# Kernel optimization log

Hardware: AMD Instinct MI355X
Metric: run time of the kernel (lower is better)

The kernel has to match this reference:

```python
import jax, jax.numpy as jnp
import numpy as np
import math

B, N, H, D = 2, 2048, 16, 64

def setup_inputs() -> dict:
    key = jax.random.key(0)
    kq, kk, kv = jax.random.split(key, 3)
    q = jax.random.normal(kq, (B, N, H, D), dtype=jnp.float32)
    k = jax.random.normal(kk, (B, N, H, D), dtype=jnp.float32)
    v = jax.random.normal(kv, (B, N, H, D), dtype=jnp.float32)
    return {"q": q, "k": k, "v": v}

def reference(q, k, v):
    d = q.shape[-1]
    # [b,n,h,d] -> [b,h,n,d]
    qh = jnp.transpose(q, (0, 2, 1, 3))
    kh = jnp.transpose(k, (0, 2, 1, 3))
    vh = jnp.transpose(v, (0, 2, 1, 3))
    # scores: [b,h,n,n]
    scores = jnp.einsum('bhqd,bhkd->bhqk', qh, kh) / math.sqrt(d)
    # jax.nn.softmax performs the stable max-subtraction internally,
    # matching the original's explicit max-subtract + softmax.
    attn = jax.nn.softmax(scores, axis=-1)
    o = jnp.einsum('bhqk,bhkd->bhqd', attn, vh)
    # back to [b,n,h,d]
    return jnp.transpose(o, (0, 2, 1, 3))
```

## Files before the change

### kernel.cpp

```cpp
#include <hip/hip_runtime.h>


typedef float  f32x4  __attribute__((ext_vector_type(4)));
typedef float  f32x16 __attribute__((ext_vector_type(16)));
typedef short  s16x8  __attribute__((ext_vector_type(8)));
typedef short  s16x4  __attribute__((ext_vector_type(4)));
typedef int    i32x4  __attribute__((ext_vector_type(4)));

#define QSCALE 0.18033688011112042f

__device__ __forceinline__ unsigned short bf16r(float f) {
    unsigned u = __builtin_bit_cast(unsigned, f);
    u += 0x7fffu + ((u >> 16) & 1u);
    return (unsigned short)(u >> 16);
}

__device__ __forceinline__ s16x8 cvt8f(const float* p) {
    f32x4 a = *(const f32x4*)p;
    f32x4 b = *(const f32x4*)(p + 4);
    s16x8 r;
#pragma unroll
    for (int i = 0; i < 4; ++i) { r[i] = (short)bf16r(a[i]); r[i+4] = (short)bf16r(b[i]); }
    return r;
}

__device__ __forceinline__ s16x8 cvt8f_scaled(const float* p, float s) {
    f32x4 a = *(const f32x4*)p;
    f32x4 b = *(const f32x4*)(p + 4);
    s16x8 r;
#pragma unroll
    for (int i = 0; i < 4; ++i) {
        r[i]   = (short)bf16r(a[i] * s);
        r[i+4] = (short)bf16r(b[i] * s);
    }
    return r;
}

__device__ __forceinline__ void gll16(const unsigned short* g, short* l) {
    __builtin_amdgcn_global_load_lds(
        (const __attribute__((address_space(1))) unsigned int*)g,
        (__attribute__((address_space(3))) unsigned int*)l, 16, 0, 0);
}

__device__ __forceinline__ int pack2(float lo, float hi) {
    unsigned ul = __builtin_bit_cast(unsigned, lo) + 0x8000u;
    unsigned uh = __builtin_bit_cast(unsigned, hi) + 0x8000u;
    return (int)__builtin_amdgcn_perm(uh, ul, 0x07060302u);
}

__global__ void __launch_bounds__(256)
prep(const float* __restrict__ K, const float* __restrict__ V,
     unsigned short* __restrict__ Kb, unsigned short* __restrict__ Vt) {
    const int t = threadIdx.x, bid = blockIdx.x;
    {
        size_t i = ((size_t)bid * 256 + t) * 16;
        *(s16x8*)(Kb + i)     = cvt8f(K + i);
        *(s16x8*)(Kb + i + 8) = cvt8f(K + i + 8);
    }
    __shared__ short tile[64 * 72];
    const int bh = bid & 31, nb = bid >> 5;
    const int b = bh >> 4, h = bh & 15;
    {
        const int l16 = t & 15, r = t >> 4;
#pragma unroll
        for (int p = 0; p < 4; ++p) {
            const int nl = p * 16 + r;
            const float* vp = V + ((size_t)(b * 2048 + nb * 64 + nl)) * 1024 + h * 64 + l16 * 4;
            f32x4 x = *(const f32x4*)vp;
#pragma unroll
            for (int i = 0; i < 4; ++i)
                tile[(l16 * 4 + i) * 72 + nl] = (short)bf16r(x[i]);
        }
    }
    __syncthreads();
    {
        const int s = t & 7, d0 = t >> 3;
#pragma unroll
        for (int p = 0; p < 2; ++p) {
            const int d = p * 32 + d0;
            s16x8 x = *(const s16x8*)&tile[d * 72 + s * 8];
            *(s16x8*)(Vt + ((size_t)(bh * 64 + d)) * 2048 + nb * 64 + s * 8) = x;
        }
    }
}

__global__ void __launch_bounds__(256, 2)
attn_fwd(const float* __restrict__ Q, const unsigned short* __restrict__ Kb,
         const unsigned short* __restrict__ Vt, float* __restrict__ O)
{
    __shared__ __align__(16) char smem[65536];

    const int t = threadIdx.x;
    const int w = t >> 6, lane = t & 63;
    const int g = lane >> 5, nl = lane & 31;
    const int qsel = w & 1, ksel = w >> 1;

    const int bid = blockIdx.x;
    const int bh  = bid & 31, qb = bid >> 5;
    const int b   = bh >> 4,  h  = bh & 15;
    const int q0  = qb * 128 + qsel * 64;

    s16x8 qf[2][4];
#pragma unroll
    for (int qt = 0; qt < 2; ++qt) {
        const float* qp = Q + ((size_t)(b * 2048 + q0 + qt * 32 + nl)) * 1024
                            + h * 64 + g * 8;
#pragma unroll
        for (int kc = 0; kc < 4; ++kc)
            qf[qt][kc] = cvt8f_scaled(qp + kc * 16, QSCALE);
    }

    f32x16 oa[2][2] = {};
    float lp[2] = {0.f, 0.f};

    const int lr = lane >> 3, ls = lane & 7;
    int koff[4], voff[4];
#pragma unroll
    for (int i = 0; i < 4; ++i) {
        const int r = qsel * 32 + i * 8 + lr;
        const int c = (ls - r) & 7;
        koff[i] = r * 1024 + c * 8;
        voff[i] = r * 2048 + c * 8;
    }
    const unsigned short* gKh = Kb + (size_t)b * 2097152 + h * 64;
    const unsigned short* gVh = Vt + (size_t)bh * 131072;
    short* dK[2] = { (short*)(smem + (0 * 2 + ksel) * 8192) + qsel * 2048,
                     (short*)(smem + (1 * 2 + ksel) * 8192) + qsel * 2048 };
    short* dV[2] = { (short*)(smem + 32768 + (0 * 2 + ksel) * 8192) + qsel * 2048,
                     (short*)(smem + 32768 + (1 * 2 + ksel) * 8192) + qsel * 2048 };

    auto issue = [&](int it, int buf) {
        const int kb = ksel * 16 + it;
        const unsigned short* gk = gKh + (size_t)kb * 65536;
        const unsigned short* gv = gVh + kb * 64;
#pragma unroll
        for (int i = 0; i < 4; ++i) {
            gll16(gk + koff[i], dK[buf] + i * 512);
            gll16(gv + voff[i], dV[buf] + i * 512);
        }
    };

    issue(0, 0);

    for (int it = 0; it < 16; ++it) {
        const int cur = it & 1;
        __syncthreads();
        if (it + 1 < 16) issue(it + 1, cur ^ 1);

        const short* bK = (const short*)(smem + (cur * 2 + ksel) * 8192);
        const short* bV = (const short*)(smem + 32768 + (cur * 2 + ksel) * 8192);

        int pk[2][2][8];
#pragma unroll
        for (int kt = 0; kt < 2; ++kt) {
            s16x8 af[4];
#pragma unroll
            for (int kc = 0; kc < 4; ++kc) {
                const int row = kt * 32 + nl;
                af[kc] = *(const s16x8*)&bK[row * 64 + ((2 * kc + g + row) & 7) * 8];
            }
#pragma unroll
            for (int qt = 0; qt < 2; ++qt) {
                f32x16 s = {};
#pragma unroll
                for (int kc = 0; kc < 4; ++kc)
                    s = __builtin_amdgcn_mfma_f32_32x32x16_bf16(af[kc], qf[qt][kc], s, 0, 0, 0);
                float p[16];
#pragma unroll
                for (int r = 0; r < 16; ++r) {
                    p[r] = __builtin_amdgcn_exp2f(s[r]);
                    lp[qt] += p[r];
                }
#pragma unroll
                for (int i = 0; i < 8; ++i)
                    pk[kt][qt][i] = pack2(p[2 * i], p[2 * i + 1]);
            }
        }

#pragma unroll
        for (int dt = 0; dt < 2; ++dt) {
            const int row = dt * 32 + nl;
#pragma unroll
            for (int kt = 0; kt < 2; ++kt) {
#pragma unroll
                for (int s = 0; s < 2; ++s) {
                    s16x4 aL = *(const s16x4*)&bV[row * 64 + ((4 * kt + s     + row) & 7) * 8 + g * 4];
                    s16x4 aH = *(const s16x4*)&bV[row * 64 + ((4 * kt + 2 + s + row) & 7) * 8 + g * 4];
                    s16x8 a = __builtin_shufflevector(aL, aH, 0, 1, 2, 3, 4, 5, 6, 7);
#pragma unroll
                    for (int qt = 0; qt < 2; ++qt) {
                        i32x4 bd = { pk[kt][qt][s * 2], pk[kt][qt][s * 2 + 1],
                                     pk[kt][qt][s * 2 + 4], pk[kt][qt][s * 2 + 5] };
                        oa[dt][qt] = __builtin_amdgcn_mfma_f32_32x32x16_bf16(
                            a, __builtin_bit_cast(s16x8, bd), oa[dt][qt], 0, 0, 0);
                    }
                }
            }
        }
    }

    __syncthreads();
    float* ex = (float*)smem;
    float* zone = ex + qsel * 4224 + lane * 66;
    if (ksel) {
#pragma unroll
        for (int dt = 0; dt < 2; ++dt)
#pragma unroll
            for (int qt = 0; qt < 2; ++qt)
#pragma unroll
                for (int i = 0; i < 4; ++i)
                    *(f32x4*)(zone + (dt * 2 + qt) * 16 + i * 4) =
                        (f32x4){ oa[dt][qt][4*i], oa[dt][qt][4*i+1],
                                 oa[dt][qt][4*i+2], oa[dt][qt][4*i+3] };
        zone[64] = lp[0];
        zone[65] = lp[1];
    }
    __syncthreads();
    if (!ksel) {
#pragma unroll
        for (int dt = 0; dt < 2; ++dt)
#pragma unroll
            for (int qt = 0; qt < 2; ++qt)
#pragma unroll
                for (int i = 0; i < 4; ++i) {
                    f32x4 u = *(const f32x4*)(zone + (dt * 2 + qt) * 16 + i * 4);
#pragma unroll
                    for (int j = 0; j < 4; ++j) oa[dt][qt][4*i+j] += u[j];
                }
        float inv[2];
#pragma unroll
        for (int qt = 0; qt < 2; ++qt) {
            float s = lp[qt] + zone[64 + qt];
            s += __shfl_xor(s, 32);
            inv[qt] = 1.0f / s;
        }
#pragma unroll
        for (int qt = 0; qt < 2; ++qt) {
            float* op = O + ((size_t)(b * 2048 + q0 + qt * 32 + nl)) * 1024 + h * 64;
#pragma unroll
            for (int dt = 0; dt < 2; ++dt)
#pragma unroll
                for (int rq = 0; rq < 4; ++rq) {
                    const int d = dt * 32 + 8 * rq + 4 * g;
                    *(f32x4*)(op + d) = (f32x4){
                        oa[dt][qt][4*rq]   * inv[qt], oa[dt][qt][4*rq+1] * inv[qt],
                        oa[dt][qt][4*rq+2] * inv[qt], oa[dt][qt][4*rq+3] * inv[qt] };
                }
        }
    }
}

extern "C" void kernel_launch(void* const* d_in, const int* in_sizes, int n_in,
                              void* d_out, int out_size, void* d_ws, size_t ws_size,
                              hipStream_t stream) {
    const float* q = (const float*)d_in[0];
    const float* k = (const float*)d_in[1];
    const float* v = (const float*)d_in[2];
    float* o = (float*)d_out;

    unsigned short* Kb = (unsigned short*)d_ws;
    unsigned short* Vt = Kb + 4194304;

    hipLaunchKernelGGL(prep,     dim3(1024), dim3(256), 0, stream, k, v, Kb, Vt);
    hipLaunchKernelGGL(attn_fwd, dim3(512),  dim3(256), 0, stream, q, Kb, Vt, o);
}
```

Baseline: 135.9 us.

## Pre-tile and pre-swizzle K/V in prep so each wave streams private LDS buffers

The prep kernel now writes K and V as per-head contiguous 32-key tiles that are already in the swizzled LDS layout. Each wave then owns a private double-buffered LDS region, loads it with linear global_load_lds, and waits only on its own vmcnt, so the per-iteration block-wide __syncthreads disappears. The loop now processes 32-key steps (32 iterations) and hoists K/V fragment reads ahead of the next prefetch. It also vectorises the softmax row-sum accumulation. The risks are that waves loading the same key tiles now fetch them redundantly instead of sharing, and that an LDS buffer reused right after the vmcnt wait could race between waves.

After: 134.0 us. About the same (-1.4%).

```diff
diff --git a/kernel.cpp b/kernel.cpp
--- a/kernel.cpp
+++ b/kernel.cpp
@@ -50,42 +50,51 @@
 
 __global__ void __launch_bounds__(256)
 prep(const float* __restrict__ K, const float* __restrict__ V,
-     unsigned short* __restrict__ Kb, unsigned short* __restrict__ Vt) {
+     unsigned short* __restrict__ Kt, unsigned short* __restrict__ Vt) {
     const int t = threadIdx.x, bid = blockIdx.x;
-    {
-        size_t i = ((size_t)bid * 256 + t) * 16;
-        *(s16x8*)(Kb + i)     = cvt8f(K + i);
-        *(s16x8*)(Kb + i + 8) = cvt8f(K + i + 8);
-    }
-    __shared__ short tile[64 * 72];
     const int bh = bid & 31, nb = bid >> 5;
     const int b = bh >> 4, h = bh & 15;
+    const size_t tile0 = ((size_t)bh * 64 + nb * 2) * 2048;
+
+#pragma unroll
+    for (int i = 0; i < 2; ++i) {
+        const int lin = t * 2 + i;
+        const int kbl = lin >> 8, rem = lin & 255;
+        const int r = rem >> 3, s = rem & 7;
+        const int c = (s - r) & 7;
+        const float* src = K + ((size_t)(b * 2048 + nb * 64 + kbl * 32 + r)) * 1024
+                             + h * 64 + c * 8;
+        *(s16x8*)(Kt + tile0 + kbl * 2048 + r * 64 + s * 8) = cvt8f(src);
+    }
+
+    __shared__ short tile[64 * 72];
     {
         const int l16 = t & 15, r = t >> 4;
 #pragma unroll
         for (int p = 0; p < 4; ++p) {
-            const int nl = p * 16 + r;
-            const float* vp = V + ((size_t)(b * 2048 + nb * 64 + nl)) * 1024 + h * 64 + l16 * 4;
+            const int key = p * 16 + r;
+            const float* vp = V + ((size_t)(b * 2048 + nb * 64 + key)) * 1024
+                                + h * 64 + l16 * 4;
             f32x4 x = *(const f32x4*)vp;
 #pragma unroll
             for (int i = 0; i < 4; ++i)
-                tile[(l16 * 4 + i) * 72 + nl] = (short)bf16r(x[i]);
+                tile[(l16 * 4 + i) * 72 + key] = (short)bf16r(x[i]);
         }
     }
     __syncthreads();
-    {
-        const int s = t & 7, d0 = t >> 3;
-#pragma unroll
-        for (int p = 0; p < 2; ++p) {
-            const int d = p * 32 + d0;
-            s16x8 x = *(const s16x8*)&tile[d * 72 + s * 8];
-            *(s16x8*)(Vt + ((size_t)(bh * 64 + d)) * 2048 + nb * 64 + s * 8) = x;
-        }
+#pragma unroll
+    for (int i = 0; i < 4; ++i) {
+        const int lin = t * 4 + i;
+        const int kbl = lin >> 9, rem = lin & 511;
+        const int d = rem >> 3, p = rem & 7;
+        const int u = (p - (d >> 1)) & 7;
+        s16x4 x = *(const s16x4*)&tile[d * 72 + kbl * 32 + u * 4];
+        *(s16x4*)(Vt + tile0 + kbl * 2048 + d * 32 + p * 4) = x;
     }
 }
 
 __global__ void __launch_bounds__(256, 2)
-attn_fwd(const float* __restrict__ Q, const unsigned short* __restrict__ Kb,
+attn_fwd(const float* __restrict__ Q, const unsigned short* __restrict__ Kt,
          const unsigned short* __restrict__ Vt, float* __restrict__ O)
 {
     __shared__ __align__(16) char smem[65536];
@@ -100,6 +109,10 @@
     const int b   = bh >> 4,  h  = bh & 15;
     const int q0  = qb * 128 + qsel * 64;
 
+    char* wbase = smem + w * 16384;
+    short* sKb[2] = { (short*)wbase,            (short*)(wbase + 4096) };
+    short* sVb[2] = { (short*)(wbase + 8192),   (short*)(wbase + 12288) };
+
     s16x8 qf[2][4];
 #pragma unroll
     for (int qt = 0; qt < 2; ++qt) {
@@ -110,98 +123,98 @@
             qf[qt][kc] = cvt8f_scaled(qp + kc * 16, QSCALE);
     }
 
+    int koffr[4];
+#pragma unroll
+    for (int kc = 0; kc < 4; ++kc)
+        koffr[kc] = nl * 64 + ((2 * kc + g + nl) & 7) * 8;
+    int voffr[2][2];
+#pragma unroll
+    for (int s = 0; s < 2; ++s) {
+        voffr[s][0] = nl * 32 + (((2 * s + g)     + (nl >> 1)) & 7) * 4;
+        voffr[s][1] = nl * 32 + (((4 + 2 * s + g) + (nl >> 1)) & 7) * 4;
+    }
+
+    const int lane8 = lane * 8;
+    const unsigned short* gbase = Kt + (size_t)bh * 131072;
+    const unsigned short* vbase = Vt + (size_t)bh * 131072;
+
+    auto issue = [&](int it, int buf) {
+        const int kb = ksel * 32 + it;
+        const unsigned short* gk = gbase + (size_t)kb * 2048 + lane8;
+        const unsigned short* gv = vbase + (size_t)kb * 2048 + lane8;
+#pragma unroll
+        for (int i = 0; i < 4; ++i) {
+            gll16(gk + i * 512, sKb[buf] + i * 512);
+            gll16(gv + i * 512, sVb[buf] + i * 512);
+        }
+    };
+
+    issue(0, 0);
+
     f32x16 oa[2][2] = {};
-    float lp[2] = {0.f, 0.f};
-
-    const int lr = lane >> 3, ls = lane & 7;
-    int koff[4], voff[4];
-#pragma unroll
-    for (int i = 0; i < 4; ++i) {
-        const int r = qsel * 32 + i * 8 + lr;
-        const int c = (ls - r) & 7;
-        koff[i] = r * 1024 + c * 8;
-        voff[i] = r * 2048 + c * 8;
-    }
-    const unsigned short* gKh = Kb + (size_t)b * 2097152 + h * 64;
-    const unsigned short* gVh = Vt + (size_t)bh * 131072;
-    short* dK[2] = { (short*)(smem + (0 * 2 + ksel) * 8192) + qsel * 2048,
-                     (short*)(smem + (1 * 2 + ksel) * 8192) + qsel * 2048 };
-    short* dV[2] = { (short*)(smem + 32768 + (0 * 2 + ksel) * 8192) + qsel * 2048,
-                     (short*)(smem + 32768 + (1 * 2 + ksel) * 8192) + qsel * 2048 };
-
-    auto issue = [&](int it, int buf) {
-        const int kb = ksel * 16 + it;
-        const unsigned short* gk = gKh + (size_t)kb * 65536;
-        const unsigned short* gv = gVh + kb * 64;
-#pragma unroll
-        for (int i = 0; i < 4; ++i) {
-            gll16(gk + koff[i], dK[buf] + i * 512);
-            gll16(gv + voff[i], dV[buf] + i * 512);
-        }
-    };
-
-    issue(0, 0);
-
-    for (int it = 0; it < 16; ++it) {
+    f32x4 lpv[2] = {};
+
+#pragma unroll 2
+    for (int it = 0; it < 32; ++it) {
         const int cur = it & 1;
-        __syncthreads();
-        if (it + 1 < 16) issue(it + 1, cur ^ 1);
-
-        const short* bK = (const short*)(smem + (cur * 2 + ksel) * 8192);
-        const short* bV = (const short*)(smem + 32768 + (cur * 2 + ksel) * 8192);
-
-        int pk[2][2][8];
-#pragma unroll
-        for (int kt = 0; kt < 2; ++kt) {
-            s16x8 af[4];
-#pragma unroll
-            for (int kc = 0; kc < 4; ++kc) {
-                const int row = kt * 32 + nl;
-                af[kc] = *(const s16x8*)&bK[row * 64 + ((2 * kc + g + row) & 7) * 8];
+        const short* bK = sKb[cur];
+        const short* bV = sVb[cur];
+
+        asm volatile("s_waitcnt vmcnt(0)" ::: "memory");
+
+        s16x8 kf[4];
+#pragma unroll
+        for (int kc = 0; kc < 4; ++kc) kf[kc] = *(const s16x8*)&bK[koffr[kc]];
+        s16x4 vfl[2][2], vfh[2][2];
+#pragma unroll
+        for (int dt = 0; dt < 2; ++dt)
+#pragma unroll
+            for (int s = 0; s < 2; ++s) {
+                vfl[dt][s] = *(const s16x4*)&bV[dt * 1024 + voffr[s][0]];
+                vfh[dt][s] = *(const s16x4*)&bV[dt * 1024 + voffr[s][1]];
             }
-#pragma unroll
-            for (int qt = 0; qt < 2; ++qt) {
-                f32x16 s = {};
-#pragma unroll
-                for (int kc = 0; kc < 4; ++kc)
-                    s = __builtin_amdgcn_mfma_f32_32x32x16_bf16(af[kc], qf[qt][kc], s, 0, 0, 0);
-                float p[16];
-#pragma unroll
-                for (int r = 0; r < 16; ++r) {
-                    p[r] = __builtin_amdgcn_exp2f(s[r]);
-                    lp[qt] += p[r];
-                }
-#pragma unroll
-                for (int i = 0; i < 8; ++i)
-                    pk[kt][qt][i] = pack2(p[2 * i], p[2 * i + 1]);
-            }
-        }
-
-#pragma unroll
-        for (int dt = 0; dt < 2; ++dt) {
-            const int row = dt * 32 + nl;
-#pragma unroll
-            for (int kt = 0; kt < 2; ++kt) {
-#pragma unroll
-                for (int s = 0; s < 2; ++s) {
-                    s16x4 aL = *(const s16x4*)&bV[row * 64 + ((4 * kt + s     + row) & 7) * 8 + g * 4];
-                    s16x4 aH = *(const s16x4*)&bV[row * 64 + ((4 * kt + 2 + s + row) & 7) * 8 + g * 4];
-                    s16x8 a = __builtin_shufflevector(aL, aH, 0, 1, 2, 3, 4, 5, 6, 7);
-#pragma unroll
-                    for (int qt = 0; qt < 2; ++qt) {
-                        i32x4 bd = { pk[kt][qt][s * 2], pk[kt][qt][s * 2 + 1],
-                                     pk[kt][qt][s * 2 + 4], pk[kt][qt][s * 2 + 5] };
-                        oa[dt][qt] = __builtin_amdgcn_mfma_f32_32x32x16_bf16(
-                            a, __builtin_bit_cast(s16x8, bd), oa[dt][qt], 0, 0, 0);
-                    }
+
+        if (it + 1 < 32) issue(it + 1, cur ^ 1);
+
+        int pk[2][8];
+#pragma unroll
+        for (int qt = 0; qt < 2; ++qt) {
+            f32x16 sacc = {};
+#pragma unroll
+            for (int kc = 0; kc < 4; ++kc)
+                sacc = __builtin_amdgcn_mfma_f32_32x32x16_bf16(kf[kc], qf[qt][kc], sacc, 0, 0, 0);
+            float p[16];
+#pragma unroll
+            for (int r = 0; r < 16; ++r) p[r] = __builtin_amdgcn_exp2f(sacc[r]);
+#pragma unroll
+            for (int i = 0; i < 4; ++i)
+                lpv[qt] += (f32x4){p[4*i], p[4*i+1], p[4*i+2], p[4*i+3]};
+#pragma unroll
+            for (int i = 0; i < 8; ++i) pk[qt][i] = pack2(p[2*i], p[2*i+1]);
+        }
+
+#pragma unroll
+        for (int dt = 0; dt < 2; ++dt)
+#pragma unroll
+            for (int s = 0; s < 2; ++s) {
+                s16x8 a = __builtin_shufflevector(vfl[dt][s], vfh[dt][s],
+                                                  0, 1, 2, 3, 4, 5, 6, 7);
+#pragma unroll
+                for (int qt = 0; qt < 2; ++qt) {
+                    i32x4 bd = { pk[qt][s*2], pk[qt][s*2+1],
+                                 pk[qt][s*2+4], pk[qt][s*2+5] };
+                    oa[dt][qt] = __builtin_amdgcn_mfma_f32_32x32x16_bf16(
+                        a, __builtin_bit_cast(s16x8, bd), oa[dt][qt], 0, 0, 0);
                 }
             }
-        }
-    }
+    }
+
+    float lp[2] = { lpv[0][0] + lpv[0][1] + lpv[0][2] + lpv[0][3],
+                    lpv[1][0] + lpv[1][1] + lpv[1][2] + lpv[1][3] };
 
     __syncthreads();
     float* ex = (float*)smem;
-    float* zone = ex + qsel * 4224 + lane * 66;
+    float* zone = ex + qsel * (64 * 68) + lane * 68;
     if (ksel) {
 #pragma unroll
         for (int dt = 0; dt < 2; ++dt)
@@ -210,7 +223,7 @@
 #pragma unroll
                 for (int i = 0; i < 4; ++i)
                     *(f32x4*)(zone + (dt * 2 + qt) * 16 + i * 4) =
-                        (f32x4){ oa[dt][qt][4*i], oa[dt][qt][4*i+1],
+                        (f32x4){ oa[dt][qt][4*i],   oa[dt][qt][4*i+1],
                                  oa[dt][qt][4*i+2], oa[dt][qt][4*i+3] };
         zone[64] = lp[0];
         zone[65] = lp[1];
@@ -258,9 +271,9 @@
     const float* v = (const float*)d_in[2];
     float* o = (float*)d_out;
 
-    unsigned short* Kb = (unsigned short*)d_ws;
-    unsigned short* Vt = Kb + 4194304;
-
-    hipLaunchKernelGGL(prep,     dim3(1024), dim3(256), 0, stream, k, v, Kb, Vt);
-    hipLaunchKernelGGL(attn_fwd, dim3(512),  dim3(256), 0, stream, q, Kb, Vt, o);
-}
+    unsigned short* Kt = (unsigned short*)d_ws;
+    unsigned short* Vt = Kt + 4194304;
+
+    hipLaunchKernelGGL(prep,     dim3(1024), dim3(256), 0, stream, k, v, Kt, Vt);
+    hipLaunchKernelGGL(attn_fwd, dim3(512),  dim3(256), 0, stream, q, Kt, Vt, o);
+}
```
